# Performance work log

Measured on AMD Instinct MI355X. Metric: run time of the kernel, lower is better.

## Reference

```python
import jax, jax.numpy as jnp
import numpy as np

N_NODES = 100000
N_EDGES = 1600000
N_REL = 4


def rgcn_conv(x, src, dst, edge_type, W, root, bias):
    """PyG RGCNConv with default aggr='mean': out_i = x_i @ root + bias
    + sum_r mean_{j in N_r(i)} (x_j @ W_r)."""
    n = x.shape[0]
    num_rel = W.shape[0]
    out_dim = W.shape[2]
    # Transform all nodes by every relation weight first (small dims -> cheap),
    # avoiding a huge [E, in, out] gathered-weight tensor.
    xW = jnp.einsum('nd,rdo->rno', x, W)          # [R, N, out]
    msg = xW[edge_type, src]                      # [E, out] gather
    seg = edge_type.astype(jnp.int32) * n + dst   # composite (relation, dst) id
    num_seg = num_rel * n
    sums = jax.ops.segment_sum(msg, seg, num_segments=num_seg)            # [R*N, out]
    cnt = jax.ops.segment_sum(jnp.ones_like(seg, dtype=x.dtype), seg,
                              num_segments=num_seg)                        # [R*N]
    mean = sums / jnp.maximum(cnt, 1.0)[:, None]
    agg = mean.reshape(num_rel, n, out_dim).sum(axis=0)                    # [N, out]
    return agg + x @ root + bias


def setup_inputs() -> dict:
    key = jax.random.key(0)
    ks = jax.random.split(key, 12)
    inp = {}
    inp['x'] = jax.random.normal(ks[0], (N_NODES, 16), dtype=jnp.float32)
    inp['edge_index'] = jax.random.randint(ks[1], (2, N_EDGES), 0, N_NODES, dtype=jnp.int32)
    inp['edge_type'] = jax.random.randint(ks[2], (N_EDGES,), 0, N_REL, dtype=jnp.int32)
    dims = [(16, 16), (16, 32), (32, 64)]
    for i, (din, dout) in enumerate(dims, start=1):
        scale = 1.0 / np.sqrt(din)
        inp[f'W{i}'] = jax.random.normal(ks[3 * i], (N_REL, din, dout), dtype=jnp.float32) * scale
        inp[f'root{i}'] = jax.random.normal(ks[3 * i + 1], (din, dout), dtype=jnp.float32) * scale
        inp[f'b{i}'] = jnp.zeros((dout,), dtype=jnp.float32)
    return inp


def reference(x, edge_index, edge_type, W1, root1, b1, W2, root2, b2, W3, root3, b3):
    src, dst = edge_index[0], edge_index[1]
    h = rgcn_conv(x, src, dst, edge_type, W1, root1, b1)
    h = jax.nn.relu(h)  # dropout is identity in eval mode
    h = rgcn_conv(h, src, dst, edge_type, W2, root2, b2)
    h = jax.nn.relu(h)
    h = rgcn_conv(h, src, dst, edge_type, W3, root3, b3)
    return h
```

## Files before the change

### kernel.cpp

```cpp
#include <hip/hip_runtime.h>
#include <hip/hip_fp16.h>

#define N_NODES 100000
#define N_EDGES 1600000
#define N_REL 4

__global__ __launch_bounds__(256) void cvt_kernel(const float* __restrict__ in,
                                                  __half* __restrict__ out,
                                                  int n4) {
  int i = blockIdx.x * 256 + threadIdx.x;
  if (i >= n4) return;
  float4 v = ((const float4*)in)[i];
  __half2* o = (__half2*)(out + (long)i * 4);
  o[0] = __floats2half2_rn(v.x, v.y);
  o[1] = __floats2half2_rn(v.z, v.w);
}

__global__ __launch_bounds__(256) void count_kernel(const int* __restrict__ dst,
                                                    const int* __restrict__ et,
                                                    int* __restrict__ cnt,
                                                    int E, int N) {
  int e = blockIdx.x * 256 + threadIdx.x;
  if (e >= E) return;
  atomicAdd(&cnt[et[e] * N + dst[e]], 1);
}

__global__ __launch_bounds__(256) void alloc_kernel(const int* __restrict__ cnt,
                                                    int* __restrict__ off,
                                                    int* __restrict__ cur,
                                                    int* __restrict__ top,
                                                    int RN) {
  __shared__ int s[256];
  __shared__ int base;
  const int i = blockIdx.x * 256 + threadIdx.x;
  const int c = (i < RN) ? cnt[i] : 0;
  s[threadIdx.x] = c;
  __syncthreads();
  for (int d = 1; d < 256; d <<= 1) {
    int v = (threadIdx.x >= d) ? s[threadIdx.x - d] : 0;
    __syncthreads();
    s[threadIdx.x] += v;
    __syncthreads();
  }
  if (threadIdx.x == 255) base = atomicAdd(top, s[255]);
  __syncthreads();
  if (i < RN) {
    int excl = base + s[threadIdx.x] - c;
    off[i] = excl;
    cur[i] = excl;
  }
}

__global__ __launch_bounds__(256) void fill_kernel(
    const int* __restrict__ src, const int* __restrict__ dst,
    const int* __restrict__ et, int* __restrict__ cur, int* __restrict__ eidx,
    int E, int N) {
  int e = blockIdx.x * 256 + threadIdx.x;
  if (e >= E) return;
  int seg = et[e] * N + dst[e];
  int pos = atomicAdd(&cur[seg], 1);
  eidx[pos] = src[e];
}

template <int DIN, int DOUT, bool RELU, bool OUT_HALF>
__global__ __launch_bounds__(256, 8) void gather_transform_kernel(
    const __half* __restrict__ xh, const int* __restrict__ cnt,
    const int* __restrict__ off, const int* __restrict__ eidx,
    const float* __restrict__ W, const float* __restrict__ root,
    const float* __restrict__ bias, void* __restrict__ outp, int N) {
  constexpr int G = DIN / 8;
  constexpr int GN = 256 / (N_REL * G);
  __shared__ float sAgg[GN][N_REL][DIN];
  __shared__ float sX[GN][DIN];

  {
    const int g = threadIdx.x % G;
    const int r = (threadIdx.x / G) % N_REL;
    const int ni = threadIdx.x / (G * N_REL);
    const int node = blockIdx.x * GN + ni;
    if (node < N) {
      const float4* xv = (const float4*)xh;
      if (r == 0) {
        union { float4 f; __half2 h[4]; } u;
        u.f = xv[(long)node * G + g];
        float* d = &sX[ni][g * 8];
#pragma unroll
        for (int k = 0; k < 4; k++) {
          float2 f2 = __half22float2(u.h[k]);
          d[2 * k] = f2.x;
          d[2 * k + 1] = f2.y;
        }
      }
      const int seg = r * N + node;
      const int c = cnt[seg];
      const int st = off[seg];
      float s[8] = {0.f, 0.f, 0.f, 0.f, 0.f, 0.f, 0.f, 0.f};
      int e = 0;
      for (; e + 2 <= c; e += 2) {
        int s0 = eidx[st + e], s1 = eidx[st + e + 1];
        union { float4 f; __half2 h[4]; } u0, u1;
        u0.f = xv[(long)s0 * G + g];
        u1.f = xv[(long)s1 * G + g];
#pragma unroll
        for (int k = 0; k < 4; k++) {
          float2 a = __half22float2(u0.h[k]);
          float2 b = __half22float2(u1.h[k]);
          s[2 * k] += a.x + b.x;
          s[2 * k + 1] += a.y + b.y;
        }
      }
      if (e < c) {
        union { float4 f; __half2 h[4]; } u0;
        u0.f = xv[(long)eidx[st + e] * G + g];
#pragma unroll
        for (int k = 0; k < 4; k++) {
          float2 a = __half22float2(u0.h[k]);
          s[2 * k] += a.x;
          s[2 * k + 1] += a.y;
        }
      }
      const float ic = (c > 0) ? 1.f / (float)c : 0.f;
      float* d = &sAgg[ni][r][g * 8];
#pragma unroll
      for (int k = 0; k < 8; k++) d[k] = s[k] * ic;
    }
  }
  __syncthreads();

  constexpr int NPP = 256 / DOUT;
  constexpr int PASSES = GN / NPP;
  const int oc = threadIdx.x % DOUT;
  const int nj0 = threadIdx.x / DOUT;
#pragma unroll
  for (int p = 0; p < PASSES; p++) {
    const int nj = nj0 + p * NPP;
    const int node2 = blockIdx.x * GN + nj;
    if (node2 < N) {
      float acc = bias[oc];
#pragma unroll
      for (int k = 0; k < DIN; k++) acc += sX[nj][k] * root[k * DOUT + oc];
#pragma unroll
      for (int r = 0; r < N_REL; r++) {
#pragma unroll
        for (int k = 0; k < DIN; k++)
          acc += sAgg[nj][r][k] * W[(r * DIN + k) * DOUT + oc];
      }
      if (RELU) acc = fmaxf(acc, 0.f);
      if (OUT_HALF)
        ((__half*)outp)[(long)node2 * DOUT + oc] = __float2half(acc);
      else
        ((float*)outp)[(long)node2 * DOUT + oc] = acc;
    }
  }
}

static inline size_t align256(size_t v) { return (v + 255) & ~(size_t)255; }

extern "C" void kernel_launch(void* const* d_in, const int* in_sizes, int n_in,
                              void* d_out, int out_size, void* d_ws,
                              size_t ws_size, hipStream_t stream) {
  const int N = N_NODES;
  const int E = N_EDGES;
  const int RN = N_REL * N;

  const float* x = (const float*)d_in[0];
  const int* edge_index = (const int*)d_in[1];
  const int* et = (const int*)d_in[2];
  const float* W1 = (const float*)d_in[3];
  const float* root1 = (const float*)d_in[4];
  const float* b1 = (const float*)d_in[5];
  const float* W2 = (const float*)d_in[6];
  const float* root2 = (const float*)d_in[7];
  const float* b2 = (const float*)d_in[8];
  const float* W3 = (const float*)d_in[9];
  const float* root3 = (const float*)d_in[10];
  const float* b3 = (const float*)d_in[11];

  const int* src = edge_index;
  const int* dst = edge_index + E;

  char* ws = (char*)d_ws;
  size_t off_b = 0;
  int* cnt = (int*)(ws + off_b);
  off_b = align256(off_b + (size_t)RN * 4);
  int* off = (int*)(ws + off_b);
  off_b = align256(off_b + (size_t)RN * 4);
  int* cur = (int*)(ws + off_b);
  off_b = align256(off_b + (size_t)RN * 4);
  int* top = (int*)(ws + off_b);
  off_b = align256(off_b + 256);
  int* eidx = (int*)(ws + off_b);
  off_b = align256(off_b + (size_t)E * 4);
  __half* xh = (__half*)(ws + off_b);
  off_b = align256(off_b + (size_t)N * 16 * 2);
  __half* h1 = (__half*)(ws + off_b);
  off_b = align256(off_b + (size_t)N * 16 * 2);
  __half* h2 = (__half*)(ws + off_b);
  off_b = align256(off_b + (size_t)N * 32 * 2);
  (void)ws_size;

  float* out = (float*)d_out;

  hipMemsetAsync(cnt, 0, (size_t)RN * 4, stream);
  hipMemsetAsync(top, 0, 256, stream);
  cvt_kernel<<<(N * 16 / 4 + 255) / 256, 256, 0, stream>>>(x, xh, N * 16 / 4);
  count_kernel<<<(E + 255) / 256, 256, 0, stream>>>(dst, et, cnt, E, N);
  alloc_kernel<<<(RN + 255) / 256, 256, 0, stream>>>(cnt, off, cur, top, RN);
  fill_kernel<<<(E + 255) / 256, 256, 0, stream>>>(src, dst, et, cur, eidx, E,
                                                   N);

  {
    constexpr int GN = 256 / (N_REL * 2);
    gather_transform_kernel<16, 16, true, true>
        <<<(N + GN - 1) / GN, 256, 0, stream>>>(xh, cnt, off, eidx, W1, root1,
                                                b1, h1, N);
  }
  {
    constexpr int GN = 256 / (N_REL * 2);
    gather_transform_kernel<16, 32, true, true>
        <<<(N + GN - 1) / GN, 256, 0, stream>>>(h1, cnt, off, eidx, W2, root2,
                                                b2, h2, N);
  }
  {
    constexpr int GN = 256 / (N_REL * 4);
    gather_transform_kernel<32, 64, false, false>
        <<<(N + GN - 1) / GN, 256, 0, stream>>>(h2, cnt, off, eidx, W3, root3,
                                                b3, out, N);
  }
}
```

Baseline: 516.5 us.

## Materialize per-edge gathered features and split wide layers into 16-wide column passes

Adds an expand kernel that gathers source-node features into a CSR-ordered per-edge buffer, so the reduction reads them contiguously instead of going through indirect eidx lookups. The 32-wide layer-2 output is stored as two 16-column halves, and layer 3 runs as two passes, the second accumulating into the float output. This turns random gathers into sequential streams, but it adds an extra 51MB write plus read per pass and four expand launches. The layer-3 split also re-reads and rewrites the output.

```diff
diff --git a/kernel.cpp b/kernel.cpp
--- a/kernel.cpp
+++ b/kernel.cpp
@@ -62,27 +62,39 @@
   eidx[pos] = src[e];
 }
 
-template <int DIN, int DOUT, bool RELU, bool OUT_HALF>
-__global__ __launch_bounds__(256, 8) void gather_transform_kernel(
-    const __half* __restrict__ xh, const int* __restrict__ cnt,
-    const int* __restrict__ off, const int* __restrict__ eidx,
-    const float* __restrict__ W, const float* __restrict__ root,
-    const float* __restrict__ bias, void* __restrict__ outp, int N) {
-  constexpr int G = DIN / 8;
-  constexpr int GN = 256 / (N_REL * G);
-  __shared__ float sAgg[GN][N_REL][DIN];
-  __shared__ float sX[GN][DIN];
+__global__ __launch_bounds__(256) void expand_kernel(
+    const __half* __restrict__ tab, const int* __restrict__ eidx,
+    __half* __restrict__ xe, int E) {
+  int t = blockIdx.x * 256 + threadIdx.x;
+  if (t >= 2 * E) return;
+  int p = t >> 1;
+  int g = t & 1;
+  int idx = eidx[p];
+  ((float4*)xe)[t] = ((const float4*)tab)[((long)idx << 1) | g];
+}
+
+template <int DOUT, bool RELU, bool ACCUM, bool SPLIT_OUT, bool OUT_HALF>
+__global__ __launch_bounds__(256, 8) void reduce_kernel(
+    const __half* __restrict__ tab,
+    const __half* __restrict__ xe,
+    const int* __restrict__ cnt, const int* __restrict__ off,
+    const float* __restrict__ W, int relStride,
+    const float* __restrict__ root,
+    const float* __restrict__ bias,
+    void* __restrict__ outA, void* __restrict__ outB, int N) {
+  constexpr int GN = 32;
+  __shared__ float sAgg[GN][N_REL][16];
+  __shared__ float sX[GN][16];
 
   {
-    const int g = threadIdx.x % G;
-    const int r = (threadIdx.x / G) % N_REL;
-    const int ni = threadIdx.x / (G * N_REL);
+    const int g = threadIdx.x & 1;
+    const int r = (threadIdx.x >> 1) & 3;
+    const int ni = threadIdx.x >> 3;
     const int node = blockIdx.x * GN + ni;
     if (node < N) {
-      const float4* xv = (const float4*)xh;
       if (r == 0) {
         union { float4 f; __half2 h[4]; } u;
-        u.f = xv[(long)node * G + g];
+        u.f = ((const float4*)tab)[((long)node << 1) | g];
         float* d = &sX[ni][g * 8];
 #pragma unroll
         for (int k = 0; k < 4; k++) {
@@ -93,25 +105,29 @@
       }
       const int seg = r * N + node;
       const int c = cnt[seg];
-      const int st = off[seg];
+      const long st = off[seg];
+      const float4* base = (const float4*)xe + (st << 1) + g;
       float s[8] = {0.f, 0.f, 0.f, 0.f, 0.f, 0.f, 0.f, 0.f};
       int e = 0;
-      for (; e + 2 <= c; e += 2) {
-        int s0 = eidx[st + e], s1 = eidx[st + e + 1];
-        union { float4 f; __half2 h[4]; } u0, u1;
-        u0.f = xv[(long)s0 * G + g];
-        u1.f = xv[(long)s1 * G + g];
+      for (; e + 4 <= c; e += 4) {
+        union { float4 f; __half2 h[4]; } u0, u1, u2, u3;
+        u0.f = base[2 * (e + 0)];
+        u1.f = base[2 * (e + 1)];
+        u2.f = base[2 * (e + 2)];
+        u3.f = base[2 * (e + 3)];
 #pragma unroll
         for (int k = 0; k < 4; k++) {
           float2 a = __half22float2(u0.h[k]);
           float2 b = __half22float2(u1.h[k]);
-          s[2 * k] += a.x + b.x;
-          s[2 * k + 1] += a.y + b.y;
+          float2 cc = __half22float2(u2.h[k]);
+          float2 dd = __half22float2(u3.h[k]);
+          s[2 * k] += (a.x + b.x) + (cc.x + dd.x);
+          s[2 * k + 1] += (a.y + b.y) + (cc.y + dd.y);
         }
       }
-      if (e < c) {
+      for (; e < c; e++) {
         union { float4 f; __half2 h[4]; } u0;
-        u0.f = xv[(long)eidx[st + e] * G + g];
+        u0.f = base[2 * e];
 #pragma unroll
         for (int k = 0; k < 4; k++) {
           float2 a = __half22float2(u0.h[k]);
@@ -136,20 +152,28 @@
     const int nj = nj0 + p * NPP;
     const int node2 = blockIdx.x * GN + nj;
     if (node2 < N) {
-      float acc = bias[oc];
-#pragma unroll
-      for (int k = 0; k < DIN; k++) acc += sX[nj][k] * root[k * DOUT + oc];
+      float acc = ACCUM ? ((const float*)outA)[(long)node2 * DOUT + oc]
+                        : bias[oc];
+#pragma unroll
+      for (int k = 0; k < 16; k++) acc += sX[nj][k] * root[k * DOUT + oc];
 #pragma unroll
       for (int r = 0; r < N_REL; r++) {
 #pragma unroll
-        for (int k = 0; k < DIN; k++)
-          acc += sAgg[nj][r][k] * W[(r * DIN + k) * DOUT + oc];
+        for (int k = 0; k < 16; k++)
+          acc += sAgg[nj][r][k] * W[r * relStride + k * DOUT + oc];
       }
       if (RELU) acc = fmaxf(acc, 0.f);
-      if (OUT_HALF)
-        ((__half*)outp)[(long)node2 * DOUT + oc] = __float2half(acc);
-      else
-        ((float*)outp)[(long)node2 * DOUT + oc] = acc;
+      if (SPLIT_OUT) {
+        __half hv = __float2half(acc);
+        if (oc < 16)
+          ((__half*)outA)[(long)node2 * 16 + oc] = hv;
+        else
+          ((__half*)outB)[(long)node2 * 16 + (oc - 16)] = hv;
+      } else if (OUT_HALF) {
+        ((__half*)outA)[(long)node2 * DOUT + oc] = __float2half(acc);
+      } else {
+        ((float*)outA)[(long)node2 * DOUT + oc] = acc;
+      }
     }
   }
 }
@@ -180,51 +204,55 @@
   const int* dst = edge_index + E;
 
   char* ws = (char*)d_ws;
-  size_t off_b = 0;
-  int* cnt = (int*)(ws + off_b);
-  off_b = align256(off_b + (size_t)RN * 4);
-  int* off = (int*)(ws + off_b);
-  off_b = align256(off_b + (size_t)RN * 4);
-  int* cur = (int*)(ws + off_b);
-  off_b = align256(off_b + (size_t)RN * 4);
-  int* top = (int*)(ws + off_b);
-  off_b = align256(off_b + 256);
-  int* eidx = (int*)(ws + off_b);
-  off_b = align256(off_b + (size_t)E * 4);
-  __half* xh = (__half*)(ws + off_b);
-  off_b = align256(off_b + (size_t)N * 16 * 2);
-  __half* h1 = (__half*)(ws + off_b);
-  off_b = align256(off_b + (size_t)N * 16 * 2);
-  __half* h2 = (__half*)(ws + off_b);
-  off_b = align256(off_b + (size_t)N * 32 * 2);
+  size_t o = 0;
+  int* cnt = (int*)(ws + o);
+  o = align256(o + (size_t)RN * 4);
+  int* off = (int*)(ws + o);
+  o = align256(o + (size_t)RN * 4);
+  int* cur = (int*)(ws + o);
+  o = align256(o + (size_t)RN * 4);
+  int* top = (int*)(ws + o);
+  o = align256(o + 256);
+  int* eidx = (int*)(ws + o);
+  o = align256(o + (size_t)E * 4);
+  __half* xh = (__half*)(ws + o);
+  o = align256(o + (size_t)N * 16 * 2);
+  __half* h1 = (__half*)(ws + o);
+  o = align256(o + (size_t)N * 16 * 2);
+  __half* h2lo = (__half*)(ws + o);
+  o = align256(o + (size_t)N * 16 * 2);
+  __half* h2hi = (__half*)(ws + o);
+  o = align256(o + (size_t)N * 16 * 2);
+  __half* xe = (__half*)(ws + o);
+  o = align256(o + (size_t)E * 16 * 2);
   (void)ws_size;
 
   float* out = (float*)d_out;
+
+  const int gridE = (E + 255) / 256;
+  const int gridX = (2 * E + 255) / 256;
+  const int gridR = (N + 31) / 32;
 
   hipMemsetAsync(cnt, 0, (size_t)RN * 4, stream);
   hipMemsetAsync(top, 0, 256, stream);
   cvt_kernel<<<(N * 16 / 4 + 255) / 256, 256, 0, stream>>>(x, xh, N * 16 / 4);
-  count_kernel<<<(E + 255) / 256, 256, 0, stream>>>(dst, et, cnt, E, N);
+  count_kernel<<<gridE, 256, 0, stream>>>(dst, et, cnt, E, N);
   alloc_kernel<<<(RN + 255) / 256, 256, 0, stream>>>(cnt, off, cur, top, RN);
-  fill_kernel<<<(E + 255) / 256, 256, 0, stream>>>(src, dst, et, cur, eidx, E,
-                                                   N);
-
-  {
-    constexpr int GN = 256 / (N_REL * 2);
-    gather_transform_kernel<16, 16, true, true>
-        <<<(N + GN - 1) / GN, 256, 0, stream>>>(xh, cnt, off, eidx, W1, root1,
-                                                b1, h1, N);
-  }
-  {
-    constexpr int GN = 256 / (N_REL * 2);
-    gather_transform_kernel<16, 32, true, true>
-        <<<(N + GN - 1) / GN, 256, 0, stream>>>(h1, cnt, off, eidx, W2, root2,
-                                                b2, h2, N);
-  }
-  {
-    constexpr int GN = 256 / (N_REL * 4);
-    gather_transform_kernel<32, 64, false, false>
-        <<<(N + GN - 1) / GN, 256, 0, stream>>>(h2, cnt, off, eidx, W3, root3,
-                                                b3, out, N);
-  }
-}
+  fill_kernel<<<gridE, 256, 0, stream>>>(src, dst, et, cur, eidx, E, N);
+
+  expand_kernel<<<gridX, 256, 0, stream>>>(xh, eidx, xe, E);
+  reduce_kernel<16, true, false, false, true><<<gridR, 256, 0, stream>>>(
+      xh, xe, cnt, off, W1, 16 * 16, root1, b1, h1, nullptr, N);
+
+  expand_kernel<<<gridX, 256, 0, stream>>>(h1, eidx, xe, E);
+  reduce_kernel<32, true, false, true, true><<<gridR, 256, 0, stream>>>(
+      h1, xe, cnt, off, W2, 16 * 32, root2, b2, h2lo, h2hi, N);
+
+  expand_kernel<<<gridX, 256, 0, stream>>>(h2lo, eidx, xe, E);
+  reduce_kernel<64, false, false, false, false><<<gridR, 256, 0, stream>>>(
+      h2lo, xe, cnt, off, W3, 32 * 64, root3, b3, out, nullptr, N);
+  expand_kernel<<<gridX, 256, 0, stream>>>(h2hi, eidx, xe, E);
+  reduce_kernel<64, false, true, false, false><<<gridR, 256, 0, stream>>>(
+      h2hi, xe, cnt, off, W3 + 16 * 64, 32 * 64, root3 + 16 * 64, nullptr, out,
+      nullptr, N);
+}
```

New measurement: 657.6 us. 27.3% more time.

## Replace atomic-offset CSR with ordered global scan and edge-parallel LDS-atomic aggregation

Applied to the files above, without the earlier changes.

Swaps the atomic bump allocator for a three-kernel ordered exclusive scan, so segments for consecutive nodes within a relation are contiguous in the edge array. Each layer kernel can then process a block of 32 nodes by walking the whole edge range per relation edge-parallel across lanes. Features are accumulated into shared memory with float atomics instead of one thread looping per segment. This is meant to remove load imbalance and serial per-segment loops from skewed degrees, at the cost of LDS atomic contention, an extra ndst array to read and write, and two extra launches.

```diff
diff --git a/kernel.cpp b/kernel.cpp
--- a/kernel.cpp
+++ b/kernel.cpp
@@ -25,116 +25,160 @@
   atomicAdd(&cnt[et[e] * N + dst[e]], 1);
 }
 
-__global__ __launch_bounds__(256) void alloc_kernel(const int* __restrict__ cnt,
-                                                    int* __restrict__ off,
-                                                    int* __restrict__ cur,
-                                                    int* __restrict__ top,
-                                                    int RN) {
+__global__ __launch_bounds__(256) void blocksum_kernel(
+    const int* __restrict__ cnt, int* __restrict__ bsum, int RN) {
   __shared__ int s[256];
-  __shared__ int base;
-  const int i = blockIdx.x * 256 + threadIdx.x;
-  const int c = (i < RN) ? cnt[i] : 0;
+  int i = blockIdx.x * 256 + threadIdx.x;
+  s[threadIdx.x] = (i < RN) ? cnt[i] : 0;
+  __syncthreads();
+  for (int d = 128; d > 0; d >>= 1) {
+    if (threadIdx.x < d) s[threadIdx.x] += s[threadIdx.x + d];
+    __syncthreads();
+  }
+  if (threadIdx.x == 0) bsum[blockIdx.x] = s[0];
+}
+
+__global__ __launch_bounds__(256) void scanb_kernel(const int* __restrict__ bsum,
+                                                    int* __restrict__ bbase,
+                                                    int nB) {
+  __shared__ int s[256];
+  __shared__ int carry;
+  if (threadIdx.x == 0) carry = 0;
+  __syncthreads();
+  for (int base = 0; base < nB; base += 256) {
+    int i = base + threadIdx.x;
+    int v = (i < nB) ? bsum[i] : 0;
+    s[threadIdx.x] = v;
+    __syncthreads();
+    for (int d = 1; d < 256; d <<= 1) {
+      int t = (threadIdx.x >= d) ? s[threadIdx.x - d] : 0;
+      __syncthreads();
+      s[threadIdx.x] += t;
+      __syncthreads();
+    }
+    if (i < nB) bbase[i] = carry + s[threadIdx.x] - v;
+    __syncthreads();
+    if (threadIdx.x == 255) carry += s[255];
+    __syncthreads();
+  }
+}
+
+__global__ __launch_bounds__(256) void alloc_kernel(
+    const int* __restrict__ cnt, const int* __restrict__ bbase,
+    int* __restrict__ off, int* __restrict__ cur, int RN, int E) {
+  __shared__ int s[256];
+  int i = blockIdx.x * 256 + threadIdx.x;
+  int c = (i < RN) ? cnt[i] : 0;
   s[threadIdx.x] = c;
   __syncthreads();
   for (int d = 1; d < 256; d <<= 1) {
-    int v = (threadIdx.x >= d) ? s[threadIdx.x - d] : 0;
-    __syncthreads();
-    s[threadIdx.x] += v;
-    __syncthreads();
-  }
-  if (threadIdx.x == 255) base = atomicAdd(top, s[255]);
-  __syncthreads();
+    int t = (threadIdx.x >= d) ? s[threadIdx.x - d] : 0;
+    __syncthreads();
+    s[threadIdx.x] += t;
+    __syncthreads();
+  }
   if (i < RN) {
-    int excl = base + s[threadIdx.x] - c;
-    off[i] = excl;
-    cur[i] = excl;
-  }
+    int ex = bbase[blockIdx.x] + s[threadIdx.x] - c;
+    off[i] = ex;
+    cur[i] = ex;
+  }
+  if (i == 0) off[RN] = E;
 }
 
 __global__ __launch_bounds__(256) void fill_kernel(
     const int* __restrict__ src, const int* __restrict__ dst,
     const int* __restrict__ et, int* __restrict__ cur, int* __restrict__ eidx,
-    int E, int N) {
+    int* __restrict__ ndst, int E, int N) {
   int e = blockIdx.x * 256 + threadIdx.x;
   if (e >= E) return;
-  int seg = et[e] * N + dst[e];
+  int d = dst[e];
+  int seg = et[e] * N + d;
   int pos = atomicAdd(&cur[seg], 1);
   eidx[pos] = src[e];
+  ndst[pos] = d;
 }
 
 template <int DIN, int DOUT, bool RELU, bool OUT_HALF>
-__global__ __launch_bounds__(256, 8) void gather_transform_kernel(
-    const __half* __restrict__ xh, const int* __restrict__ cnt,
+__global__ __launch_bounds__(256, 8) void rgcn_layer_kernel(
+    const __half* __restrict__ tab, const int* __restrict__ cnt,
     const int* __restrict__ off, const int* __restrict__ eidx,
-    const float* __restrict__ W, const float* __restrict__ root,
-    const float* __restrict__ bias, void* __restrict__ outp, int N) {
-  constexpr int G = DIN / 8;
-  constexpr int GN = 256 / (N_REL * G);
-  __shared__ float sAgg[GN][N_REL][DIN];
-  __shared__ float sX[GN][DIN];
-
-  {
-    const int g = threadIdx.x % G;
-    const int r = (threadIdx.x / G) % N_REL;
-    const int ni = threadIdx.x / (G * N_REL);
-    const int node = blockIdx.x * GN + ni;
+    const int* __restrict__ ndst, const float* __restrict__ W,
+    const float* __restrict__ root, const float* __restrict__ bias,
+    void* __restrict__ outp, int N) {
+  constexpr int GRAN = DIN / 8;
+  constexpr int NB = 32;
+  __shared__ float sAgg[NB][N_REL][DIN];
+  __shared__ float sX[NB][DIN];
+  const int tid = threadIdx.x;
+  const int n0 = blockIdx.x * NB;
+
+  for (int i = tid; i < NB * N_REL * DIN; i += 256) (&sAgg[0][0][0])[i] = 0.f;
+  if (tid < NB * GRAN) {
+    int nl = tid / GRAN, g = tid % GRAN;
+    int node = n0 + nl;
     if (node < N) {
-      const float4* xv = (const float4*)xh;
-      if (r == 0) {
+      union { float4 f; __half2 h[4]; } u;
+      u.f = ((const float4*)tab)[(long)node * GRAN + g];
+      float* d = &sX[nl][g * 8];
+#pragma unroll
+      for (int k = 0; k < 4; k++) {
+        float2 f2 = __half22float2(u.h[k]);
+        d[2 * k] = f2.x;
+        d[2 * k + 1] = f2.y;
+      }
+    }
+  }
+  __syncthreads();
+
+  const int wid = tid >> 6, lane = tid & 63;
+  const int gg = wid % GRAN;
+  const int chunk = wid / GRAN;
+  constexpr int CHUNKS = 4 / GRAN;
+#pragma unroll
+  for (int r = 0; r < N_REL; r++) {
+    int nend = n0 + NB;
+    if (nend > N) nend = N;
+    const int pStart = off[r * N + n0];
+    const int pEnd = off[r * N + nend];
+    for (int p0 = pStart + chunk * 64; p0 < pEnd; p0 += CHUNKS * 64) {
+      const int p = p0 + lane;
+      if (p < pEnd) {
+        const int sidx = eidx[p];
+        const int nl = ndst[p] - n0;
         union { float4 f; __half2 h[4]; } u;
-        u.f = xv[(long)node * G + g];
-        float* d = &sX[ni][g * 8];
+        u.f = ((const float4*)tab)[(long)sidx * GRAN + gg];
+        float* d = &sAgg[nl][r][gg * 8];
 #pragma unroll
         for (int k = 0; k < 4; k++) {
           float2 f2 = __half22float2(u.h[k]);
-          d[2 * k] = f2.x;
-          d[2 * k + 1] = f2.y;
+          atomicAdd(&d[2 * k], f2.x);
+          atomicAdd(&d[2 * k + 1], f2.y);
         }
       }
-      const int seg = r * N + node;
-      const int c = cnt[seg];
-      const int st = off[seg];
-      float s[8] = {0.f, 0.f, 0.f, 0.f, 0.f, 0.f, 0.f, 0.f};
-      int e = 0;
-      for (; e + 2 <= c; e += 2) {
-        int s0 = eidx[st + e], s1 = eidx[st + e + 1];
-        union { float4 f; __half2 h[4]; } u0, u1;
-        u0.f = xv[(long)s0 * G + g];
-        u1.f = xv[(long)s1 * G + g];
-#pragma unroll
-        for (int k = 0; k < 4; k++) {
-          float2 a = __half22float2(u0.h[k]);
-          float2 b = __half22float2(u1.h[k]);
-          s[2 * k] += a.x + b.x;
-          s[2 * k + 1] += a.y + b.y;
-        }
-      }
-      if (e < c) {
-        union { float4 f; __half2 h[4]; } u0;
-        u0.f = xv[(long)eidx[st + e] * G + g];
-#pragma unroll
-        for (int k = 0; k < 4; k++) {
-          float2 a = __half22float2(u0.h[k]);
-          s[2 * k] += a.x;
-          s[2 * k + 1] += a.y;
-        }
-      }
+    }
+  }
+  __syncthreads();
+
+  if (tid < NB * N_REL) {
+    const int nl = tid >> 2, r = tid & 3;
+    const int node = n0 + nl;
+    if (node < N) {
+      const int c = cnt[r * N + node];
       const float ic = (c > 0) ? 1.f / (float)c : 0.f;
-      float* d = &sAgg[ni][r][g * 8];
-#pragma unroll
-      for (int k = 0; k < 8; k++) d[k] = s[k] * ic;
+#pragma unroll
+      for (int ch = 0; ch < DIN; ch++) sAgg[nl][r][ch] *= ic;
     }
   }
   __syncthreads();
 
   constexpr int NPP = 256 / DOUT;
-  constexpr int PASSES = GN / NPP;
-  const int oc = threadIdx.x % DOUT;
-  const int nj0 = threadIdx.x / DOUT;
+  constexpr int PASSES = NB / NPP;
+  const int oc = tid % DOUT;
+  const int nj0 = tid / DOUT;
 #pragma unroll
   for (int p = 0; p < PASSES; p++) {
     const int nj = nj0 + p * NPP;
-    const int node2 = blockIdx.x * GN + nj;
+    const int node2 = n0 + nj;
     if (node2 < N) {
       float acc = bias[oc];
 #pragma unroll
@@ -162,6 +206,7 @@
   const int N = N_NODES;
   const int E = N_EDGES;
   const int RN = N_REL * N;
+  const int nB = (RN + 255) / 256;
 
   const float* x = (const float*)d_in[0];
   const int* edge_index = (const int*)d_in[1];
@@ -180,51 +225,46 @@
   const int* dst = edge_index + E;
 
   char* ws = (char*)d_ws;
-  size_t off_b = 0;
-  int* cnt = (int*)(ws + off_b);
-  off_b = align256(off_b + (size_t)RN * 4);
-  int* off = (int*)(ws + off_b);
-  off_b = align256(off_b + (size_t)RN * 4);
-  int* cur = (int*)(ws + off_b);
-  off_b = align256(off_b + (size_t)RN * 4);
-  int* top = (int*)(ws + off_b);
-  off_b = align256(off_b + 256);
-  int* eidx = (int*)(ws + off_b);
-  off_b = align256(off_b + (size_t)E * 4);
-  __half* xh = (__half*)(ws + off_b);
-  off_b = align256(off_b + (size_t)N * 16 * 2);
-  __half* h1 = (__half*)(ws + off_b);
-  off_b = align256(off_b + (size_t)N * 16 * 2);
-  __half* h2 = (__half*)(ws + off_b);
-  off_b = align256(off_b + (size_t)N * 32 * 2);
+  size_t o = 0;
+  int* cnt = (int*)(ws + o);
+  o = align256(o + (size_t)RN * 4);
+  int* off = (int*)(ws + o);
+  o = align256(o + (size_t)(RN + 1) * 4);
+  int* cur = (int*)(ws + o);
+  o = align256(o + (size_t)RN * 4);
+  int* bsum = (int*)(ws + o);
+  o = align256(o + (size_t)nB * 4);
+  int* bbase = (int*)(ws + o);
+  o = align256(o + (size_t)nB * 4);
+  int* eidx = (int*)(ws + o);
+  o = align256(o + (size_t)E * 4);
+  int* ndst = (int*)(ws + o);
+  o = align256(o + (size_t)E * 4);
+  __half* xh = (__half*)(ws + o);
+  o = align256(o + (size_t)N * 16 * 2);
+  __half* h1 = (__half*)(ws + o);
+  o = align256(o + (size_t)N * 16 * 2);
+  __half* h2 = (__half*)(ws + o);
+  o = align256(o + (size_t)N * 32 * 2);
   (void)ws_size;
 
   float* out = (float*)d_out;
 
+  const int gridE = (E + 255) / 256;
+  const int gridL = N / 32;
+
   hipMemsetAsync(cnt, 0, (size_t)RN * 4, stream);
-  hipMemsetAsync(top, 0, 256, stream);
   cvt_kernel<<<(N * 16 / 4 + 255) / 256, 256, 0, stream>>>(x, xh, N * 16 / 4);
-  count_kernel<<<(E + 255) / 256, 256, 0, stream>>>(dst, et, cnt, E, N);
-  alloc_kernel<<<(RN + 255) / 256, 256, 0, stream>>>(cnt, off, cur, top, RN);
-  fill_kernel<<<(E + 255) / 256, 256, 0, stream>>>(src, dst, et, cur, eidx, E,
-                                                   N);
-
-  {
-    constexpr int GN = 256 / (N_REL * 2);
-    gather_transform_kernel<16, 16, true, true>
-        <<<(N + GN - 1) / GN, 256, 0, stream>>>(xh, cnt, off, eidx, W1, root1,
-                                                b1, h1, N);
-  }
-  {
-    constexpr int GN = 256 / (N_REL * 2);
-    gather_transform_kernel<16, 32, true, true>
-        <<<(N + GN - 1) / GN, 256, 0, stream>>>(h1, cnt, off, eidx, W2, root2,
-                                                b2, h2, N);
-  }
-  {
-    constexpr int GN = 256 / (N_REL * 4);
-    gather_transform_kernel<32, 64, false, false>
-        <<<(N + GN - 1) / GN, 256, 0, stream>>>(h2, cnt, off, eidx, W3, root3,
-                                                b3, out, N);
-  }
-}
+  count_kernel<<<gridE, 256, 0, stream>>>(dst, et, cnt, E, N);
+  blocksum_kernel<<<nB, 256, 0, stream>>>(cnt, bsum, RN);
+  scanb_kernel<<<1, 256, 0, stream>>>(bsum, bbase, nB);
+  alloc_kernel<<<nB, 256, 0, stream>>>(cnt, bbase, off, cur, RN, E);
+  fill_kernel<<<gridE, 256, 0, stream>>>(src, dst, et, cur, eidx, ndst, E, N);
+
+  rgcn_layer_kernel<16, 16, true, true><<<gridL, 256, 0, stream>>>(
+      xh, cnt, off, eidx, ndst, W1, root1, b1, h1, N);
+  rgcn_layer_kernel<16, 32, true, true><<<gridL, 256, 0, stream>>>(
+      h1, cnt, off, eidx, ndst, W2, root2, b2, h2, N);
+  rgcn_layer_kernel<32, 64, false, false><<<gridL, 256, 0, stream>>>(
+      h2, cnt, off, eidx, ndst, W3, root3, b3, out, N);
+}
```

Result: slower. 1.073 ms (+107.7%).
